# Optimization experiments

Measured on AMD Instinct MI355X. Metric: run time of the kernel, lower is better.

## Reference

```python
import jax, jax.numpy as jnp
import numpy as np
from jax import lax

N, D, K = 4096, 64, 5


def setup_inputs() -> dict:
    key = jax.random.key(0)
    k1, k2 = jax.random.split(key)
    x = jax.random.normal(k1, (N, D), dtype=jnp.float32)
    y = jax.random.normal(k2, (N, D), dtype=jnp.float32)
    kernel_scales = jnp.array([0.5, 1.0, 2.0, 4.0, 8.0], dtype=jnp.float32)
    return {"x": x, "y": y, "kernel_scales": kernel_scales}


def _sqdist(a, b):
    # squared euclidean pairwise distances: [Na, Nb]
    an = jnp.sum(a * a, axis=1)
    bn = jnp.sum(b * b, axis=1)
    return an[:, None] + bn[None, :] - 2.0 * (a @ b.T)


def _median_lower(m):
    # torch.median on even-sized flattened tensor returns the LOWER middle element
    f = m.reshape(-1)
    return jnp.sort(f)[(f.size - 1) // 2]


def _kernel_sum(dist, scale):
    # multi-bandwidth RBF: mean over K kernels (default weights = 1/K each)
    # dist: [N, M], scale: [K]  ->  [N, M]
    return jnp.mean(jnp.exp(dist[:, :, None] * scale), axis=2)


def reference(x, y, kernel_scales):
    xx = _sqdist(x, x)
    yy = _sqdist(y, y)
    zz = _sqdist(x, y)
    # scale = -1/median(xx), computed under no_grad in the original
    base_scale = lax.stop_gradient(-1.0 / _median_lower(xx))
    scale = base_scale * kernel_scales  # [K]

    kxx = _kernel_sum(xx, scale)
    kyy = _kernel_sum(yy, scale)
    kzz = _kernel_sum(zz, scale)

    n = xx.shape[0]
    diag = jnp.arange(n)
    kxx = kxx.at[diag, diag].set(0.0)
    kyy = kyy.at[diag, diag].set(0.0)

    off_diag = 1.0 / (n * (n - 1))
    return off_diag * jnp.sum(kxx) + off_diag * jnp.sum(kyy) - 2.0 * jnp.mean(kzz)
```

## Files before the change

kernel.cpp:

```cpp
#include <hip/hip_runtime.h>

#define NN 4096
#define DD 64
#define KK 5
#define NBINS 1024
#define BINMUL 2.0f
#define RMED 8388607u
#define MBUF_CAP 8192u

typedef short short8 __attribute__((ext_vector_type(8)));
typedef float f32x4 __attribute__((ext_vector_type(4)));

struct Ctrl {
  unsigned wcount;
  unsigned wover;
  unsigned gcount;
  unsigned sel_bin;
  unsigned rank;
  unsigned ok;
  unsigned wrank;
  unsigned spref;
  unsigned srank;
  unsigned use_pow;
  float median;
  float c2;
  float scales[KK];
};

__device__ inline float fast_exp2(float x) {
  float r;
  asm("v_exp_f32 %0, %1" : "=v"(r) : "v"(x));
  return r;
}
__device__ inline unsigned short bf16_rn(float f) {
  unsigned u = __float_as_uint(f);
  return (unsigned short)((u + 0x7FFFu + ((u >> 16) & 1u)) >> 16);
}
__device__ inline float bf16_val(unsigned short h) {
  return __uint_as_float(((unsigned)h) << 16);
}

__global__ void __launch_bounds__(256)
split_kernel(const float* __restrict__ x, const float* __restrict__ y,
             short* __restrict__ xhi, short* __restrict__ xlo,
             short* __restrict__ yhi, short* __restrict__ ylo) {
  unsigned tid = blockIdx.x * 256u + threadIdx.x;
  unsigned e = tid * 4u;
  const float* src;
  short *dhi, *dlo;
  unsigned local;
  if (e < (unsigned)(NN * DD)) { src = x; dhi = xhi; dlo = xlo; local = e; }
  else { src = y; dhi = yhi; dlo = ylo; local = e - NN * DD; }
  float4 v = *(const float4*)(src + local);
  unsigned short h0 = bf16_rn(v.x), h1 = bf16_rn(v.y), h2 = bf16_rn(v.z), h3 = bf16_rn(v.w);
  unsigned short l0 = bf16_rn(v.x - bf16_val(h0));
  unsigned short l1 = bf16_rn(v.y - bf16_val(h1));
  unsigned short l2 = bf16_rn(v.z - bf16_val(h2));
  unsigned short l3 = bf16_rn(v.w - bf16_val(h3));
  unsigned long long H = (unsigned long long)h0 | ((unsigned long long)h1 << 16) |
                         ((unsigned long long)h2 << 32) | ((unsigned long long)h3 << 48);
  unsigned long long L = (unsigned long long)l0 | ((unsigned long long)l1 << 16) |
                         ((unsigned long long)l2 << 32) | ((unsigned long long)l3 << 48);
  *(unsigned long long*)((char*)dhi + (size_t)local * 2) = H;
  *(unsigned long long*)((char*)dlo + (size_t)local * 2) = L;
}

__global__ void norms_kernel(const float* __restrict__ x, const float* __restrict__ y,
                             float* __restrict__ xn, float* __restrict__ yn) {
  int r = blockIdx.x * blockDim.x + threadIdx.x;
  const float* src = (r < NN) ? x : y;
  float* dst = (r < NN) ? xn : yn;
  int row = r & (NN - 1);
  const float4* p = (const float4*)(src + (size_t)row * DD);
  float s = 0.f;
#pragma unroll
  for (int i = 0; i < DD / 4; ++i) {
    float4 v = p[i];
    s = fmaf(v.x, v.x, s);
    s = fmaf(v.y, v.y, s);
    s = fmaf(v.z, v.z, s);
    s = fmaf(v.w, v.w, s);
  }
  dst[row] = s;
}

template <int MODE>
__global__ void __launch_bounds__(256)
pair_kernel(const short* __restrict__ xhi, const short* __restrict__ xlo,
            const short* __restrict__ yhi, const short* __restrict__ ylo,
            const float* __restrict__ xn, const float* __restrict__ yn,
            unsigned* __restrict__ hist, Ctrl* __restrict__ ctrl,
            float* __restrict__ buf, double* __restrict__ S,
            int lobin, int hibin, unsigned cap) {
  if (MODE == 1) {
    if (ctrl->ok) return;
  }
  __shared__ __align__(16) char smem[65536];
  char* As = smem;
  char* Bs = smem + 32768;

  int t = threadIdx.x;
  int sel = (MODE == 2) ? blockIdx.z : 0;
  const short* Ah = (sel == 1) ? yhi : xhi;
  const short* Al = (sel == 1) ? ylo : xlo;
  const short* Bh = (sel == 0) ? xhi : yhi;
  const short* Bl = (sel == 0) ? xlo : ylo;
  const float* An = (sel == 1) ? yn : xn;
  const float* Bn = (sel == 0) ? xn : yn;

  int rowBase = blockIdx.y * 128;
  int colBase = blockIdx.x * 128;

  int lane = t & 63, wid = t >> 6;
  int wr = (wid >> 1) * 64, wc = (wid & 1) * 64;
  int lrow = lane & 15;
  int lk8 = (lane >> 4) * 8;
  int lswz = (lane & 7) << 4;

  {
    const char* gAh = (const char*)Ah + (size_t)rowBase * 128;
    const char* gAl = (const char*)Al + (size_t)rowBase * 128;
    const char* gBh = (const char*)Bh + (size_t)colBase * 128;
    const char* gBl = (const char*)Bl + (size_t)colBase * 128;
    short8 rAh[4], rAl[4], rBh[4], rBl[4];
#pragma unroll
    for (int i = 0; i < 4; ++i) {
      int o = t * 16 + i * 4096;
      rAh[i] = *(const short8*)(gAh + o);
      rAl[i] = *(const short8*)(gAl + o);
      rBh[i] = *(const short8*)(gBh + o);
      rBl[i] = *(const short8*)(gBl + o);
    }
#pragma unroll
    for (int i = 0; i < 4; ++i) {
      int o = t * 16 + i * 4096;
      int rr = o >> 7;
      int cc = (o >> 4) & 7;
      int db = (rr * 256 + cc * 16) ^ ((rr & 7) << 4);
      *(short8*)(As + db) = rAh[i];
      *(short8*)(As + db + 128) = rAl[i];
      *(short8*)(Bs + db) = rBh[i];
      *(short8*)(Bs + db + 128) = rBl[i];
    }
  }
  __syncthreads();

  f32x4 acc[4][4] = {};
#pragma unroll
  for (int kc = 0; kc < 2; ++kc) {
    short8 ah[4], al[4], bh[4], bl[4];
#pragma unroll
    for (int m = 0; m < 4; ++m) {
      int by = ((wr + m * 16 + lrow) * 256 + (lk8 + kc * 32) * 2) ^ lswz;
      ah[m] = *(const short8*)(As + by);
      al[m] = *(const short8*)(As + by + 128);
    }
#pragma unroll
    for (int n = 0; n < 4; ++n) {
      int by = ((wc + n * 16 + lrow) * 256 + (lk8 + kc * 32) * 2) ^ lswz;
      bh[n] = *(const short8*)(Bs + by);
      bl[n] = *(const short8*)(Bs + by + 128);
    }
#pragma unroll
    for (int m = 0; m < 4; ++m)
#pragma unroll
      for (int n = 0; n < 4; ++n) {
        acc[m][n] = __builtin_amdgcn_mfma_f32_16x16x32_bf16(ah[m], bh[n], acc[m][n], 0, 0, 0);
        acc[m][n] = __builtin_amdgcn_mfma_f32_16x16x32_bf16(ah[m], bl[n], acc[m][n], 0, 0, 0);
        acc[m][n] = __builtin_amdgcn_mfma_f32_16x16x32_bf16(al[m], bh[n], acc[m][n], 0, 0, 0);
      }
  }

  float anv[16], bnv[4];
#pragma unroll
  for (int m = 0; m < 4; ++m)
#pragma unroll
    for (int r = 0; r < 4; ++r)
      anv[m * 4 + r] = An[rowBase + wr + m * 16 + (lane >> 4) * 4 + r];
#pragma unroll
  for (int n = 0; n < 4; ++n) bnv[n] = Bn[colBase + wc + n * 16 + lrow];

  __syncthreads();

  if (MODE == 0 || MODE == 1) {
    unsigned* h = (unsigned*)Bs;
    float* mbuf = (float*)As;
    __shared__ unsigned bcnt, gbase;
    if (MODE == 0)
      for (int i = t; i < NBINS; i += 256) h[i] = 0;
    if (t == 0) bcnt = 0;
    __syncthreads();
    unsigned sb = (MODE == 1) ? ctrl->sel_bin : 0u;
#pragma unroll
    for (int m = 0; m < 4; ++m)
#pragma unroll
      for (int n = 0; n < 4; ++n)
#pragma unroll
        for (int r = 0; r < 4; ++r) {
          float d = (anv[m * 4 + r] + bnv[n]) - 2.0f * acc[m][n][r];
          int b = (int)(d * BINMUL);
          b = min(max(b, 0), NBINS - 1);
          if (MODE == 0) {
            atomicAdd(&h[b], 1u);
            if (b >= lobin && b < hibin) {
              unsigned idx = atomicAdd(&bcnt, 1u);
              if (idx < MBUF_CAP) mbuf[idx] = d - 100.0f;
              else ctrl->wover = 1u;
            }
          } else {
            if ((unsigned)b == sb) {
              unsigned idx = atomicAdd(&bcnt, 1u);
              if (idx < MBUF_CAP) mbuf[idx] = d - 100.0f;
            }
          }
        }
    __syncthreads();
    if (MODE == 0)
      for (int i = t; i < NBINS; i += 256)
        if (h[i]) atomicAdd(&hist[i], h[i]);
    unsigned cnt = min(bcnt, MBUF_CAP);
    if (t == 0) gbase = atomicAdd(MODE == 0 ? &ctrl->wcount : &ctrl->gcount, cnt);
    __syncthreads();
    for (unsigned i = t; i < cnt; i += 256) {
      unsigned gi = gbase + i;
      if (gi < cap) buf[gi] = mbuf[i];
    }
  }

  if (MODE == 2) {
    float s = 0.f;
    if (ctrl->use_pow) {
      float c2 = ctrl->c2;
#pragma unroll
      for (int m = 0; m < 4; ++m)
#pragma unroll
        for (int n = 0; n < 4; ++n)
#pragma unroll
          for (int r = 0; r < 4; ++r) {
            float d = (anv[m * 4 + r] + bnv[n]) - 2.0f * acc[m][n][r];
            float u = fast_exp2(d * c2);
            float u2 = u * u, u4 = u2 * u2, u8 = u4 * u4, u16 = u8 * u8;
            s += ((u + u2) + (u4 + u8)) + u16;
          }
    } else {
      float sc[KK];
#pragma unroll
      for (int k = 0; k < KK; ++k) sc[k] = ctrl->scales[k];
#pragma unroll
      for (int m = 0; m < 4; ++m)
#pragma unroll
        for (int n = 0; n < 4; ++n)
#pragma unroll
          for (int r = 0; r < 4; ++r) {
            float d = (anv[m * 4 + r] + bnv[n]) - 2.0f * acc[m][n][r];
            float e = 0.f;
#pragma unroll
            for (int k = 0; k < KK; ++k) e += expf(d * sc[k]);
            s += e;
          }
    }
    double sd = (double)s;
#pragma unroll
    for (int off = 32; off > 0; off >>= 1) sd += __shfl_down(sd, off);
    double* wsum = (double*)As;
    if ((t & 63) == 0) wsum[wid] = sd;
    __syncthreads();
    if (t == 0) atomicAdd(&S[sel], (wsum[0] + wsum[1]) + (wsum[2] + wsum[3]));
  }
}

__global__ void __launch_bounds__(256)
select_bin_kernel(const unsigned* __restrict__ hist, Ctrl* __restrict__ ctrl,
                  int lobin, int hibin, unsigned cap) {
  __shared__ unsigned ps[256];
  __shared__ unsigned s_cumlo;
  int t = threadIdx.x;
  unsigned loc[NBINS / 256];
  unsigned s = 0;
#pragma unroll
  for (int i = 0; i < NBINS / 256; ++i) {
    loc[i] = hist[t * (NBINS / 256) + i];
    s += loc[i];
  }
  ps[t] = s;
  __syncthreads();
  for (int off = 1; off < 256; off <<= 1) {
    unsigned v = ps[t];
    unsigned add = (t >= off) ? ps[t - off] : 0u;
    __syncthreads();
    ps[t] = v + add;
    __syncthreads();
  }
  unsigned incl = ps[t], excl = incl - s;
  if (t == (lobin >> 2)) {
    unsigned c = excl;
    for (int i = 0; i < (lobin & 3); ++i) c += loc[i];
    s_cumlo = c;
  }
  __syncthreads();
  if (RMED >= excl && RMED < incl) {
    unsigned rank = RMED - excl;
    int bsel = -1;
#pragma unroll
    for (int i = 0; i < NBINS / 256; ++i) {
      if (bsel < 0) {
        if (rank < loc[i]) bsel = t * (NBINS / 256) + i;
        else rank -= loc[i];
      }
    }
    ctrl->sel_bin = (unsigned)bsel;
    ctrl->rank = rank;
    unsigned wrank = RMED - s_cumlo;
    unsigned ok = (bsel >= lobin && bsel < hibin && ctrl->wover == 0u &&
                   ctrl->wcount <= cap && wrank < ctrl->wcount) ? 1u : 0u;
    ctrl->wrank = wrank;
    ctrl->ok = ok;
  }
}

__global__ void __launch_bounds__(256)
radix_hist_kernel(const Ctrl* __restrict__ ctrl, const float* __restrict__ buf,
                  unsigned* __restrict__ gh, int round, unsigned cap) {
  __shared__ unsigned h[256];
  int t = threadIdx.x;
  h[t] = 0;
  __syncthreads();
  unsigned m = min(ctrl->ok ? ctrl->wcount : ctrl->gcount, cap);
  int shift = 24 - 8 * round;
  unsigned pref = ctrl->spref;
  for (unsigned i = blockIdx.x * 256u + t; i < m; i += gridDim.x * 256u) {
    unsigned u = __float_as_uint(buf[i]);
    u ^= (u >> 31) ? 0xFFFFFFFFu : 0x80000000u;
    bool ok = (round == 0) || (((u ^ pref) >> (shift + 8)) == 0u);
    if (ok) atomicAdd(&h[(u >> shift) & 255u], 1u);
  }
  __syncthreads();
  if (h[t]) atomicAdd(&gh[round * 256 + t], h[t]);
}

__global__ void __launch_bounds__(256)
radix_scan_kernel(Ctrl* __restrict__ ctrl, const unsigned* __restrict__ gh,
                  const float* __restrict__ ksc, int round) {
  __shared__ unsigned ps[256];
  int t = threadIdx.x;
  unsigned rank = (round == 0) ? (ctrl->ok ? ctrl->wrank : ctrl->rank) : ctrl->srank;
  unsigned c = gh[round * 256 + t];
  ps[t] = c;
  __syncthreads();
  for (int off = 1; off < 256; off <<= 1) {
    unsigned v = ps[t];
    unsigned add = (t >= off) ? ps[t - off] : 0u;
    __syncthreads();
    ps[t] = v + add;
    __syncthreads();
  }
  unsigned incl = ps[t], excl = incl - c;
  if (rank >= excl && rank < incl) {
    int shift = 24 - 8 * round;
    unsigned np = ctrl->spref | ((unsigned)t << shift);
    ctrl->spref = np;
    ctrl->srank = rank - excl;
    if (round == 3) {
      unsigned u = (np & 0x80000000u) ? (np ^ 0x80000000u) : ~np;
      float med = __uint_as_float(u) + 100.0f;
      ctrl->median = med;
      float base = -1.0f / med;
#pragma unroll
      for (int k = 0; k < KK; ++k) ctrl->scales[k] = base * ksc[k];
      ctrl->c2 = base * 0.5f * 1.44269504088896f;
      ctrl->use_pow = (ksc[0] == 0.5f && ksc[1] == 1.0f && ksc[2] == 2.0f &&
                       ksc[3] == 4.0f && ksc[4] == 8.0f) ? 1u : 0u;
    }
  }
}

__global__ void finalize_kernel(const double* __restrict__ S, float* __restrict__ out) {
  if (threadIdx.x == 0 && blockIdx.x == 0) {
    double offd = 1.0 / ((double)NN * (double)(NN - 1));
    double invK = 1.0 / (double)KK;
    double kxx = (S[0] * invK) - (double)NN;
    double kyy = (S[1] * invK) - (double)NN;
    double kzz = S[2] * invK;
    double val = offd * (kxx + kyy) - 2.0 * kzz / ((double)NN * (double)NN);
    out[0] = (float)val;
  }
}

extern "C" void kernel_launch(void* const* d_in, const int* in_sizes, int n_in,
                              void* d_out, int out_size, void* d_ws, size_t ws_size,
                              hipStream_t stream) {
  const float* x = (const float*)d_in[0];
  const float* y = (const float*)d_in[1];
  const float* ksc = (const float*)d_in[2];

  char* ws = (char*)d_ws;
  double* S = (double*)ws;
  unsigned* hist = (unsigned*)(ws + 64);
  unsigned* gh = (unsigned*)(ws + 4160);
  Ctrl* ctrl = (Ctrl*)(ws + 8256);
  float* xn = (float*)(ws + 8384);
  float* yn = xn + NN;
  const size_t SPL = (size_t)NN * DD * 2;
  short* xhi = (short*)(ws + 65536);
  short* xlo = (short*)(ws + 65536 + SPL);
  short* yhi = (short*)(ws + 65536 + 2 * SPL);
  short* ylo = (short*)(ws + 65536 + 3 * SPL);
  size_t bufoff = 65536 + 4 * SPL;
  float* buf = (float*)(ws + bufoff);

  size_t avail = (ws_size > bufoff) ? (ws_size - bufoff) / 4 : 0;
  unsigned cap = (unsigned)((avail < (size_t)(8u << 20)) ? avail : (size_t)(8u << 20));
  int lobin, hibin;
  if (cap >= 1400000u)      { lobin = 252; hibin = 259; }
  else if (cap >= 900000u)  { lobin = 253; hibin = 258; }
  else if (cap >= 600000u)  { lobin = 254; hibin = 257; }
  else                      { lobin = 254; hibin = 256; }

  hipMemsetAsync(ws, 0, 8384, stream);

  split_kernel<<<512, 256, 0, stream>>>(x, y, xhi, xlo, yhi, ylo);
  norms_kernel<<<32, 256, 0, stream>>>(x, y, xn, yn);
  pair_kernel<0><<<dim3(32, 32), 256, 0, stream>>>(xhi, xlo, yhi, ylo, xn, yn,
                                                   hist, ctrl, buf, S, lobin, hibin, cap);
  select_bin_kernel<<<1, 256, 0, stream>>>(hist, ctrl, lobin, hibin, cap);
  pair_kernel<1><<<dim3(32, 32), 256, 0, stream>>>(xhi, xlo, yhi, ylo, xn, yn,
                                                   hist, ctrl, buf, S, lobin, hibin, cap);
  for (int r = 0; r < 4; ++r) {
    radix_hist_kernel<<<192, 256, 0, stream>>>(ctrl, buf, gh, r, cap);
    radix_scan_kernel<<<1, 256, 0, stream>>>(ctrl, gh, ksc, r);
  }
  pair_kernel<2><<<dim3(32, 32, 3), 256, 0, stream>>>(xhi, xlo, yhi, ylo, xn, yn,
                                                      hist, ctrl, buf, S, lobin, hibin, cap);
  finalize_kernel<<<1, 64, 0, stream>>>(S, (float*)d_out);
}
```

Before: 198.3 us.

## Fuse split/norms, fold scans into last-block, replace histogram pass with below-count window check

Merges the bf16 split and row-norm kernels into one launch and folds the radix scan and bin selection into the last block of each histogram kernel using a ticket counter, which removes several tiny single-block launches. The first pair pass now counts elements below a float window and copies in-window values instead of building a full histogram. A separate histogram pass (mode 3) runs only when that window check fails. LDS staging moves to a padded 80-byte row layout loaded in two K halves, and the exp argument is folded into FMAs. The trade-offs are ticket-based last-block synchronisation and possibly more LDS bank conflicts from the padded layout.

```diff
diff --git a/kernel.cpp b/kernel.cpp
--- a/kernel.cpp
+++ b/kernel.cpp
@@ -6,7 +6,9 @@
 #define NBINS 1024
 #define BINMUL 2.0f
 #define RMED 8388607u
-#define MBUF_CAP 8192u
+#define ROWB 80
+#define TILEB (128 * ROWB)
+#define MBUF_FLOATS 10240u
 
 typedef short short8 __attribute__((ext_vector_type(8)));
 typedef float f32x4 __attribute__((ext_vector_type(4)));
@@ -14,11 +16,10 @@
 struct Ctrl {
   unsigned wcount;
   unsigned wover;
+  unsigned below;
   unsigned gcount;
   unsigned sel_bin;
   unsigned rank;
-  unsigned ok;
-  unsigned wrank;
   unsigned spref;
   unsigned srank;
   unsigned use_pow;
@@ -27,6 +28,10 @@
   float scales[KK];
 };
 
+__device__ inline bool window_ok(const Ctrl* c, unsigned cap) {
+  return (c->wover == 0u) && (c->wcount <= cap) && (c->below <= RMED) &&
+         ((RMED - c->below) < c->wcount);
+}
 __device__ inline float fast_exp2(float x) {
   float r;
   asm("v_exp_f32 %0, %1" : "=v"(r) : "v"(x));
@@ -41,17 +46,15 @@
 }
 
 __global__ void __launch_bounds__(256)
-split_kernel(const float* __restrict__ x, const float* __restrict__ y,
-             short* __restrict__ xhi, short* __restrict__ xlo,
-             short* __restrict__ yhi, short* __restrict__ ylo) {
-  unsigned tid = blockIdx.x * 256u + threadIdx.x;
-  unsigned e = tid * 4u;
-  const float* src;
-  short *dhi, *dlo;
-  unsigned local;
-  if (e < (unsigned)(NN * DD)) { src = x; dhi = xhi; dlo = xlo; local = e; }
-  else { src = y; dhi = yhi; dlo = ylo; local = e - NN * DD; }
-  float4 v = *(const float4*)(src + local);
+splitnorms_kernel(const float* __restrict__ x, const float* __restrict__ y,
+                  short* __restrict__ xhi, short* __restrict__ xlo,
+                  short* __restrict__ yhi, short* __restrict__ ylo,
+                  float* __restrict__ xn, float* __restrict__ yn) {
+  unsigned g = blockIdx.x * 256u + threadIdx.x;
+  const float* src; short *dhi, *dlo; float* nrm; unsigned local;
+  if (g < 65536u) { src = x; dhi = xhi; dlo = xlo; nrm = xn; local = g; }
+  else { src = y; dhi = yhi; dlo = ylo; nrm = yn; local = g - 65536u; }
+  float4 v = *(const float4*)(src + (size_t)local * 4);
   unsigned short h0 = bf16_rn(v.x), h1 = bf16_rn(v.y), h2 = bf16_rn(v.z), h3 = bf16_rn(v.w);
   unsigned short l0 = bf16_rn(v.x - bf16_val(h0));
   unsigned short l1 = bf16_rn(v.y - bf16_val(h1));
@@ -61,27 +64,15 @@
                          ((unsigned long long)h2 << 32) | ((unsigned long long)h3 << 48);
   unsigned long long L = (unsigned long long)l0 | ((unsigned long long)l1 << 16) |
                          ((unsigned long long)l2 << 32) | ((unsigned long long)l3 << 48);
-  *(unsigned long long*)((char*)dhi + (size_t)local * 2) = H;
-  *(unsigned long long*)((char*)dlo + (size_t)local * 2) = L;
-}
-
-__global__ void norms_kernel(const float* __restrict__ x, const float* __restrict__ y,
-                             float* __restrict__ xn, float* __restrict__ yn) {
-  int r = blockIdx.x * blockDim.x + threadIdx.x;
-  const float* src = (r < NN) ? x : y;
-  float* dst = (r < NN) ? xn : yn;
-  int row = r & (NN - 1);
-  const float4* p = (const float4*)(src + (size_t)row * DD);
-  float s = 0.f;
-#pragma unroll
-  for (int i = 0; i < DD / 4; ++i) {
-    float4 v = p[i];
-    s = fmaf(v.x, v.x, s);
-    s = fmaf(v.y, v.y, s);
-    s = fmaf(v.z, v.z, s);
-    s = fmaf(v.w, v.w, s);
-  }
-  dst[row] = s;
+  *(unsigned long long*)((char*)dhi + (size_t)local * 8) = H;
+  *(unsigned long long*)((char*)dlo + (size_t)local * 8) = L;
+  float part = v.x * v.x;
+  part = fmaf(v.y, v.y, part);
+  part = fmaf(v.z, v.z, part);
+  part = fmaf(v.w, v.w, part);
+#pragma unroll
+  for (int off = 1; off < 16; off <<= 1) part += __shfl_xor(part, off);
+  if ((threadIdx.x & 15) == 0) nrm[local >> 4] = part;
 }
 
 template <int MODE>
@@ -91,85 +82,72 @@
             const float* __restrict__ xn, const float* __restrict__ yn,
             unsigned* __restrict__ hist, Ctrl* __restrict__ ctrl,
             float* __restrict__ buf, double* __restrict__ S,
-            int lobin, int hibin, unsigned cap) {
-  if (MODE == 1) {
-    if (ctrl->ok) return;
-  }
-  __shared__ __align__(16) char smem[65536];
-  char* As = smem;
-  char* Bs = smem + 32768;
+            unsigned* __restrict__ tick, float loE, float hiE, unsigned cap) {
+  if (MODE == 1 || MODE == 3) {
+    if (window_ok(ctrl, cap)) return;
+  }
+  __shared__ __align__(16) char smem[4 * TILEB];
+  __shared__ unsigned bcnt, gbase, lastflag;
 
   int t = threadIdx.x;
   int sel = (MODE == 2) ? blockIdx.z : 0;
-  const short* Ah = (sel == 1) ? yhi : xhi;
-  const short* Al = (sel == 1) ? ylo : xlo;
-  const short* Bh = (sel == 0) ? xhi : yhi;
-  const short* Bl = (sel == 0) ? xlo : ylo;
+  const char* Ah = (const char*)((sel == 1) ? yhi : xhi);
+  const char* Al = (const char*)((sel == 1) ? ylo : xlo);
+  const char* Bh = (const char*)((sel == 0) ? xhi : yhi);
+  const char* Bl = (const char*)((sel == 0) ? xlo : ylo);
   const float* An = (sel == 1) ? yn : xn;
   const float* Bn = (sel == 0) ? xn : yn;
-
-  int rowBase = blockIdx.y * 128;
-  int colBase = blockIdx.x * 128;
+  int rowBase = blockIdx.y * 128, colBase = blockIdx.x * 128;
+  const char* gsrc0 = Ah + (size_t)rowBase * 128;
+  const char* gsrc1 = Al + (size_t)rowBase * 128;
+  const char* gsrc2 = Bh + (size_t)colBase * 128;
+  const char* gsrc3 = Bl + (size_t)colBase * 128;
 
   int lane = t & 63, wid = t >> 6;
   int wr = (wid >> 1) * 64, wc = (wid & 1) * 64;
   int lrow = lane & 15;
-  int lk8 = (lane >> 4) * 8;
-  int lswz = (lane & 7) << 4;
-
-  {
-    const char* gAh = (const char*)Ah + (size_t)rowBase * 128;
-    const char* gAl = (const char*)Al + (size_t)rowBase * 128;
-    const char* gBh = (const char*)Bh + (size_t)colBase * 128;
-    const char* gBl = (const char*)Bl + (size_t)colBase * 128;
-    short8 rAh[4], rAl[4], rBh[4], rBl[4];
-#pragma unroll
-    for (int i = 0; i < 4; ++i) {
-      int o = t * 16 + i * 4096;
-      rAh[i] = *(const short8*)(gAh + o);
-      rAl[i] = *(const short8*)(gAl + o);
-      rBh[i] = *(const short8*)(gBh + o);
-      rBl[i] = *(const short8*)(gBl + o);
-    }
-#pragma unroll
-    for (int i = 0; i < 4; ++i) {
-      int o = t * 16 + i * 4096;
-      int rr = o >> 7;
-      int cc = (o >> 4) & 7;
-      int db = (rr * 256 + cc * 16) ^ ((rr & 7) << 4);
-      *(short8*)(As + db) = rAh[i];
-      *(short8*)(As + db + 128) = rAl[i];
-      *(short8*)(Bs + db) = rBh[i];
-      *(short8*)(Bs + db + 128) = rBl[i];
+  int koff = (lane >> 4) * 16;
+
+  f32x4 acc[4][4] = {};
+#pragma unroll
+  for (int p = 0; p < 2; ++p) {
+    short8 rg[8];
+#pragma unroll
+    for (int i = 0; i < 8; ++i) {
+      int c = t + i * 256;
+      const char* gs = (c < 512) ? gsrc0 : (c < 1024) ? gsrc1 : (c < 1536) ? gsrc2 : gsrc3;
+      int cr = c & 511, row = cr >> 2, kc = cr & 3;
+      rg[i] = *(const short8*)(gs + (size_t)row * 128 + p * 64 + kc * 16);
+    }
+    if (p) __syncthreads();
+#pragma unroll
+    for (int i = 0; i < 8; ++i) {
+      int c = t + i * 256;
+      int tile = c >> 9, cr = c & 511, row = cr >> 2, kc = cr & 3;
+      *(short8*)(smem + tile * TILEB + row * ROWB + kc * 16) = rg[i];
+    }
+    __syncthreads();
+    short8 bh[4], bl[4];
+#pragma unroll
+    for (int n = 0; n < 4; ++n) {
+      int off = (wc + n * 16 + lrow) * ROWB + koff;
+      bh[n] = *(const short8*)(smem + 2 * TILEB + off);
+      bl[n] = *(const short8*)(smem + 3 * TILEB + off);
+    }
+#pragma unroll
+    for (int m = 0; m < 4; ++m) {
+      int off = (wr + m * 16 + lrow) * ROWB + koff;
+      short8 ah = *(const short8*)(smem + off);
+      short8 al = *(const short8*)(smem + TILEB + off);
+#pragma unroll
+      for (int n = 0; n < 4; ++n) {
+        acc[m][n] = __builtin_amdgcn_mfma_f32_16x16x32_bf16(ah, bh[n], acc[m][n], 0, 0, 0);
+        acc[m][n] = __builtin_amdgcn_mfma_f32_16x16x32_bf16(ah, bl[n], acc[m][n], 0, 0, 0);
+        acc[m][n] = __builtin_amdgcn_mfma_f32_16x16x32_bf16(al, bh[n], acc[m][n], 0, 0, 0);
+      }
     }
   }
   __syncthreads();
-
-  f32x4 acc[4][4] = {};
-#pragma unroll
-  for (int kc = 0; kc < 2; ++kc) {
-    short8 ah[4], al[4], bh[4], bl[4];
-#pragma unroll
-    for (int m = 0; m < 4; ++m) {
-      int by = ((wr + m * 16 + lrow) * 256 + (lk8 + kc * 32) * 2) ^ lswz;
-      ah[m] = *(const short8*)(As + by);
-      al[m] = *(const short8*)(As + by + 128);
-    }
-#pragma unroll
-    for (int n = 0; n < 4; ++n) {
-      int by = ((wc + n * 16 + lrow) * 256 + (lk8 + kc * 32) * 2) ^ lswz;
-      bh[n] = *(const short8*)(Bs + by);
-      bl[n] = *(const short8*)(Bs + by + 128);
-    }
-#pragma unroll
-    for (int m = 0; m < 4; ++m)
-#pragma unroll
-      for (int n = 0; n < 4; ++n) {
-        acc[m][n] = __builtin_amdgcn_mfma_f32_16x16x32_bf16(ah[m], bh[n], acc[m][n], 0, 0, 0);
-        acc[m][n] = __builtin_amdgcn_mfma_f32_16x16x32_bf16(ah[m], bl[n], acc[m][n], 0, 0, 0);
-        acc[m][n] = __builtin_amdgcn_mfma_f32_16x16x32_bf16(al[m], bh[n], acc[m][n], 0, 0, 0);
-      }
-  }
 
   float anv[16], bnv[4];
 #pragma unroll
@@ -180,17 +158,43 @@
 #pragma unroll
   for (int n = 0; n < 4; ++n) bnv[n] = Bn[colBase + wc + n * 16 + lrow];
 
-  __syncthreads();
-
-  if (MODE == 0 || MODE == 1) {
-    unsigned* h = (unsigned*)Bs;
-    float* mbuf = (float*)As;
-    __shared__ unsigned bcnt, gbase;
-    if (MODE == 0)
-      for (int i = t; i < NBINS; i += 256) h[i] = 0;
+  if (MODE == 0) {
+    float* mbuf = (float*)smem;
     if (t == 0) bcnt = 0;
     __syncthreads();
-    unsigned sb = (MODE == 1) ? ctrl->sel_bin : 0u;
+    int below = 0;
+#pragma unroll
+    for (int m = 0; m < 4; ++m)
+#pragma unroll
+      for (int n = 0; n < 4; ++n)
+#pragma unroll
+        for (int r = 0; r < 4; ++r) {
+          float d = (anv[m * 4 + r] + bnv[n]) - 2.0f * acc[m][n][r];
+          below += (d < loE) ? 1 : 0;
+          if (d >= loE && d < hiE) {
+            unsigned idx = atomicAdd(&bcnt, 1u);
+            if (idx < MBUF_FLOATS) mbuf[idx] = d - 100.0f;
+            else ctrl->wover = 1u;
+          }
+        }
+#pragma unroll
+    for (int off = 32; off > 0; off >>= 1) below += __shfl_down(below, off);
+    if (lane == 0) atomicAdd(&ctrl->below, (unsigned)below);
+    __syncthreads();
+    unsigned cnt = min(bcnt, MBUF_FLOATS);
+    if (t == 0) gbase = atomicAdd(&ctrl->wcount, cnt);
+    __syncthreads();
+    for (unsigned i = t; i < cnt; i += 256) {
+      unsigned gi = gbase + i;
+      if (gi < cap) buf[gi] = mbuf[i];
+    }
+  }
+
+  if (MODE == 3) {
+    unsigned* h = (unsigned*)smem;
+    for (int i = t; i < NBINS; i += 256) h[i] = 0;
+    if (t == 0) lastflag = 0;
+    __syncthreads();
 #pragma unroll
     for (int m = 0; m < 4; ++m)
 #pragma unroll
@@ -200,26 +204,67 @@
           float d = (anv[m * 4 + r] + bnv[n]) - 2.0f * acc[m][n][r];
           int b = (int)(d * BINMUL);
           b = min(max(b, 0), NBINS - 1);
-          if (MODE == 0) {
-            atomicAdd(&h[b], 1u);
-            if (b >= lobin && b < hibin) {
-              unsigned idx = atomicAdd(&bcnt, 1u);
-              if (idx < MBUF_CAP) mbuf[idx] = d - 100.0f;
-              else ctrl->wover = 1u;
-            }
-          } else {
-            if ((unsigned)b == sb) {
-              unsigned idx = atomicAdd(&bcnt, 1u);
-              if (idx < MBUF_CAP) mbuf[idx] = d - 100.0f;
-            }
+          atomicAdd(&h[b], 1u);
+        }
+    __syncthreads();
+    for (int i = t; i < NBINS; i += 256)
+      if (h[i]) atomicAdd(&hist[i], h[i]);
+    __threadfence();
+    if (t == 0)
+      lastflag = (atomicAdd(&tick[4], 1u) == gridDim.x * gridDim.y - 1u) ? 1u : 0u;
+    __syncthreads();
+    if (!lastflag) return;
+    unsigned* ps = h + NBINS;
+    unsigned loc[4]; unsigned s = 0;
+#pragma unroll
+    for (int i = 0; i < 4; ++i) { loc[i] = atomicAdd(&hist[t * 4 + i], 0u); s += loc[i]; }
+    ps[t] = s;
+    __syncthreads();
+    for (int off = 1; off < 256; off <<= 1) {
+      unsigned v = ps[t];
+      unsigned add = (t >= off) ? ps[t - off] : 0u;
+      __syncthreads();
+      ps[t] = v + add;
+      __syncthreads();
+    }
+    unsigned incl = ps[t], excl = incl - s;
+    if (RMED >= excl && RMED < incl) {
+      unsigned rank = RMED - excl;
+      int bsel = -1;
+#pragma unroll
+      for (int i = 0; i < 4; ++i) {
+        if (bsel < 0) {
+          if (rank < loc[i]) bsel = t * 4 + i;
+          else rank -= loc[i];
+        }
+      }
+      ctrl->sel_bin = (unsigned)bsel;
+      ctrl->rank = rank;
+    }
+  }
+
+  if (MODE == 1) {
+    unsigned sb = ctrl->sel_bin;
+    float* mbuf = (float*)smem;
+    if (t == 0) bcnt = 0;
+    __syncthreads();
+#pragma unroll
+    for (int m = 0; m < 4; ++m)
+#pragma unroll
+      for (int n = 0; n < 4; ++n)
+#pragma unroll
+        for (int r = 0; r < 4; ++r) {
+          float d = (anv[m * 4 + r] + bnv[n]) - 2.0f * acc[m][n][r];
+          int b = (int)(d * BINMUL);
+          b = min(max(b, 0), NBINS - 1);
+          if ((unsigned)b == sb) {
+            unsigned idx = atomicAdd(&bcnt, 1u);
+            if (idx < MBUF_FLOATS) mbuf[idx] = d - 100.0f;
           }
         }
     __syncthreads();
-    if (MODE == 0)
-      for (int i = t; i < NBINS; i += 256)
-        if (h[i]) atomicAdd(&hist[i], h[i]);
-    unsigned cnt = min(bcnt, MBUF_CAP);
-    if (t == 0) gbase = atomicAdd(MODE == 0 ? &ctrl->wcount : &ctrl->gcount, cnt);
+    unsigned cnt = min(bcnt, MBUF_FLOATS);
+    if (t == 0) gbase = atomicAdd(&ctrl->gcount, cnt);
     __syncthreads();
     for (unsigned i = t; i < cnt; i += 256) {
       unsigned gi = gbase + i;
@@ -230,17 +275,25 @@
   if (MODE == 2) {
     float s = 0.f;
     if (ctrl->use_pow) {
-      float c2 = ctrl->c2;
+      float c2 = ctrl->c2, m2c2 = -2.0f * c2;
+      float bnvc[4];
+#pragma unroll
+      for (int n = 0; n < 4; ++n) bnvc[n] = bnv[n] * c2;
+#pragma unroll
+      for (int i = 0; i < 16; ++i) anv[i] *= c2;
 #pragma unroll
       for (int m = 0; m < 4; ++m)
 #pragma unroll
         for (int n = 0; n < 4; ++n)
 #pragma unroll
           for (int r = 0; r < 4; ++r) {
-            float d = (anv[m * 4 + r] + bnv[n]) - 2.0f * acc[m][n][r];
-            float u = fast_exp2(d * c2);
-            float u2 = u * u, u4 = u2 * u2, u8 = u4 * u4, u16 = u8 * u8;
-            s += ((u + u2) + (u4 + u8)) + u16;
+            float arg = fmaf(acc[m][n][r], m2c2, anv[m * 4 + r] + bnvc[n]);
+            float u = fast_exp2(arg);
+            float u2 = u * u;
+            float a = fmaf(u, u, u);
+            float u4 = u2 * u2, u8 = u4 * u4;
+            float b = fmaf(u8, u8, u8);
+            s += a; s += u4; s += b;
           }
     } else {
       float sc[KK];
@@ -262,7 +315,7 @@
     double sd = (double)s;
 #pragma unroll
     for (int off = 32; off > 0; off >>= 1) sd += __shfl_down(sd, off);
-    double* wsum = (double*)As;
+    double* wsum = (double*)smem;
     if ((t & 63) == 0) wsum[wid] = sd;
     __syncthreads();
     if (t == 0) atomicAdd(&S[sel], (wsum[0] + wsum[1]) + (wsum[2] + wsum[3]));
@@ -270,94 +323,46 @@
 }
 
 __global__ void __launch_bounds__(256)
-select_bin_kernel(const unsigned* __restrict__ hist, Ctrl* __restrict__ ctrl,
-                  int lobin, int hibin, unsigned cap) {
-  __shared__ unsigned ps[256];
-  __shared__ unsigned s_cumlo;
-  int t = threadIdx.x;
-  unsigned loc[NBINS / 256];
-  unsigned s = 0;
-#pragma unroll
-  for (int i = 0; i < NBINS / 256; ++i) {
-    loc[i] = hist[t * (NBINS / 256) + i];
-    s += loc[i];
-  }
-  ps[t] = s;
-  __syncthreads();
-  for (int off = 1; off < 256; off <<= 1) {
-    unsigned v = ps[t];
-    unsigned add = (t >= off) ? ps[t - off] : 0u;
-    __syncthreads();
-    ps[t] = v + add;
-    __syncthreads();
-  }
-  unsigned incl = ps[t], excl = incl - s;
-  if (t == (lobin >> 2)) {
-    unsigned c = excl;
-    for (int i = 0; i < (lobin & 3); ++i) c += loc[i];
-    s_cumlo = c;
-  }
-  __syncthreads();
-  if (RMED >= excl && RMED < incl) {
-    unsigned rank = RMED - excl;
-    int bsel = -1;
-#pragma unroll
-    for (int i = 0; i < NBINS / 256; ++i) {
-      if (bsel < 0) {
-        if (rank < loc[i]) bsel = t * (NBINS / 256) + i;
-        else rank -= loc[i];
-      }
-    }
-    ctrl->sel_bin = (unsigned)bsel;
-    ctrl->rank = rank;
-    unsigned wrank = RMED - s_cumlo;
-    unsigned ok = (bsel >= lobin && bsel < hibin && ctrl->wover == 0u &&
-                   ctrl->wcount <= cap && wrank < ctrl->wcount) ? 1u : 0u;
-    ctrl->wrank = wrank;
-    ctrl->ok = ok;
-  }
-}
-
-__global__ void __launch_bounds__(256)
-radix_hist_kernel(const Ctrl* __restrict__ ctrl, const float* __restrict__ buf,
-                  unsigned* __restrict__ gh, int round, unsigned cap) {
+radix_fused(Ctrl* __restrict__ ctrl, const float* __restrict__ buf,
+            unsigned* __restrict__ gh, unsigned* __restrict__ tick,
+            const float* __restrict__ ksc, int round, unsigned cap) {
   __shared__ unsigned h[256];
+  __shared__ unsigned lastflag;
   int t = threadIdx.x;
   h[t] = 0;
+  if (t == 0) lastflag = 0;
   __syncthreads();
-  unsigned m = min(ctrl->ok ? ctrl->wcount : ctrl->gcount, cap);
+  bool okw = window_ok(ctrl, cap);
+  unsigned m = min(okw ? ctrl->wcount : ctrl->gcount, cap);
+  unsigned pref = ctrl->spref;
   int shift = 24 - 8 * round;
-  unsigned pref = ctrl->spref;
   for (unsigned i = blockIdx.x * 256u + t; i < m; i += gridDim.x * 256u) {
     unsigned u = __float_as_uint(buf[i]);
     u ^= (u >> 31) ? 0xFFFFFFFFu : 0x80000000u;
-    bool ok = (round == 0) || (((u ^ pref) >> (shift + 8)) == 0u);
-    if (ok) atomicAdd(&h[(u >> shift) & 255u], 1u);
+    if (round == 0 || ((u ^ pref) >> (shift + 8)) == 0u)
+      atomicAdd(&h[(u >> shift) & 255u], 1u);
   }
   __syncthreads();
   if (h[t]) atomicAdd(&gh[round * 256 + t], h[t]);
-}
-
-__global__ void __launch_bounds__(256)
-radix_scan_kernel(Ctrl* __restrict__ ctrl, const unsigned* __restrict__ gh,
-                  const float* __restrict__ ksc, int round) {
-  __shared__ unsigned ps[256];
-  int t = threadIdx.x;
-  unsigned rank = (round == 0) ? (ctrl->ok ? ctrl->wrank : ctrl->rank) : ctrl->srank;
-  unsigned c = gh[round * 256 + t];
-  ps[t] = c;
+  __threadfence();
+  if (t == 0)
+    lastflag = (atomicAdd(&tick[round], 1u) == gridDim.x - 1u) ? 1u : 0u;
+  __syncthreads();
+  if (!lastflag) return;
+  unsigned rank = (round == 0) ? (okw ? RMED - ctrl->below : ctrl->rank) : ctrl->srank;
+  unsigned c = atomicAdd(&gh[round * 256 + t], 0u);
+  h[t] = c;
   __syncthreads();
   for (int off = 1; off < 256; off <<= 1) {
-    unsigned v = ps[t];
-    unsigned add = (t >= off) ? ps[t - off] : 0u;
-    __syncthreads();
-    ps[t] = v + add;
-    __syncthreads();
-  }
-  unsigned incl = ps[t], excl = incl - c;
+    unsigned v = h[t];
+    unsigned add = (t >= off) ? h[t - off] : 0u;
+    __syncthreads();
+    h[t] = v + add;
+    __syncthreads();
+  }
+  unsigned incl = h[t], excl = incl - c;
   if (rank >= excl && rank < incl) {
-    int shift = 24 - 8 * round;
-    unsigned np = ctrl->spref | ((unsigned)t << shift);
+    unsigned np = pref | ((unsigned)t << shift);
     ctrl->spref = np;
     ctrl->srank = rank - excl;
     if (round == 3) {
@@ -397,8 +402,9 @@
   double* S = (double*)ws;
   unsigned* hist = (unsigned*)(ws + 64);
   unsigned* gh = (unsigned*)(ws + 4160);
-  Ctrl* ctrl = (Ctrl*)(ws + 8256);
-  float* xn = (float*)(ws + 8384);
+  unsigned* tick = (unsigned*)(ws + 8256);
+  Ctrl* ctrl = (Ctrl*)(ws + 8288);
+  float* xn = (float*)(ws + 8448);
   float* yn = xn + NN;
   const size_t SPL = (size_t)NN * DD * 2;
   short* xhi = (short*)(ws + 65536);
@@ -410,26 +416,24 @@
 
   size_t avail = (ws_size > bufoff) ? (ws_size - bufoff) / 4 : 0;
   unsigned cap = (unsigned)((avail < (size_t)(8u << 20)) ? avail : (size_t)(8u << 20));
-  int lobin, hibin;
-  if (cap >= 1400000u)      { lobin = 252; hibin = 259; }
-  else if (cap >= 900000u)  { lobin = 253; hibin = 258; }
-  else if (cap >= 600000u)  { lobin = 254; hibin = 257; }
-  else                      { lobin = 254; hibin = 256; }
-
-  hipMemsetAsync(ws, 0, 8384, stream);
-
-  split_kernel<<<512, 256, 0, stream>>>(x, y, xhi, xlo, yhi, ylo);
-  norms_kernel<<<32, 256, 0, stream>>>(x, y, xn, yn);
-  pair_kernel<0><<<dim3(32, 32), 256, 0, stream>>>(xhi, xlo, yhi, ylo, xn, yn,
-                                                   hist, ctrl, buf, S, lobin, hibin, cap);
-  select_bin_kernel<<<1, 256, 0, stream>>>(hist, ctrl, lobin, hibin, cap);
-  pair_kernel<1><<<dim3(32, 32), 256, 0, stream>>>(xhi, xlo, yhi, ylo, xn, yn,
-                                                   hist, ctrl, buf, S, lobin, hibin, cap);
-  for (int r = 0; r < 4; ++r) {
-    radix_hist_kernel<<<192, 256, 0, stream>>>(ctrl, buf, gh, r, cap);
-    radix_scan_kernel<<<1, 256, 0, stream>>>(ctrl, gh, ksc, r);
-  }
-  pair_kernel<2><<<dim3(32, 32, 3), 256, 0, stream>>>(xhi, xlo, yhi, ylo, xn, yn,
-                                                      hist, ctrl, buf, S, lobin, hibin, cap);
+  float loE, hiE;
+  if (cap >= 1400000u)      { loE = 126.0f; hiE = 129.5f; }
+  else if (cap >= 900000u)  { loE = 126.5f; hiE = 129.0f; }
+  else if (cap >= 600000u)  { loE = 127.0f; hiE = 128.5f; }
+  else                      { loE = 127.0f; hiE = 128.0f; }
+
+  hipMemsetAsync(ws, 0, 8448, stream);
+
+  splitnorms_kernel<<<512, 256, 0, stream>>>(x, y, xhi, xlo, yhi, ylo, xn, yn);
+  pair_kernel<0><<<dim3(32, 32), 256, 0, stream>>>(xhi, xlo, yhi, ylo, xn, yn, hist, ctrl,
+                                                   buf, S, tick, loE, hiE, cap);
+  pair_kernel<3><<<dim3(32, 32), 256, 0, stream>>>(xhi, xlo, yhi, ylo, xn, yn, hist, ctrl,
+                                                   buf, S, tick, loE, hiE, cap);
+  pair_kernel<1><<<dim3(32, 32), 256, 0, stream>>>(xhi, xlo, yhi, ylo, xn, yn, hist, ctrl,
+                                                   buf, S, tick, loE, hiE, cap);
+  for (int r = 0; r < 4; ++r)
+    radix_fused<<<192, 256, 0, stream>>>(ctrl, buf, gh, tick, ksc, r, cap);
+  pair_kernel<2><<<dim3(32, 32, 3), 256, 0, stream>>>(xhi, xlo, yhi, ylo, xn, yn, hist, ctrl,
+                                                      buf, S, tick, loE, hiE, cap);
   finalize_kernel<<<1, 64, 0, stream>>>(S, (float*)d_out);
 }
```

Result: slower. 263.5 us (+32.9%).
